# Kernel tuning notes

Hardware: AMD Instinct MI355X
Metric: run time of the kernel (lower is better)

The kernel has to match this reference:

```python
import jax, jax.numpy as jnp
import numpy as np

B, T, C, H = 4, 2048, 2048, 16
D = C // H  # head dim = 128


def setup_inputs() -> dict:
    key = jax.random.key(0)
    k1, k2, k3, k4 = jax.random.split(key, 4)
    x = jax.random.normal(k1, (B, T, C), dtype=jnp.float32)
    # per-token key mask; force token 0 valid so no causal row is fully masked
    tok_mask = jax.random.randint(k2, (B, T), 0, 2).astype(bool).at[:, 0].set(True)
    s = 1.0 / np.sqrt(C).astype(np.float32)
    W_qkv = jax.random.normal(k3, (C, 3 * C), dtype=jnp.float32) * s
    W_proj = jax.random.normal(k4, (C, C), dtype=jnp.float32) * s
    return {"x": x, "tok_mask": tok_mask, "W_qkv": W_qkv, "W_proj": W_proj}


def reference(x, tok_mask, W_qkv, W_proj):
    Bx, Tx, Cx = x.shape
    qkv = x @ W_qkv                              # [B,T,3C]
    q, k, v = jnp.split(qkv, 3, axis=-1)
    q = q.reshape(Bx, Tx, H, D)
    k = k.reshape(Bx, Tx, H, D)
    v = v.reshape(Bx, Tx, H, D)
    scale = 1.0 / np.sqrt(D).astype(np.float32)
    scores = jnp.einsum('bqhd,bkhd->bhqk', q, k) * scale  # [B,H,T,T]
    causal = jnp.tril(jnp.ones((Tx, Tx), dtype=bool))      # [T,T]
    # tok_mask broadcasts over the query dim (key mask), AND-ed with causal
    mask = tok_mask[:, None, :] & causal                   # [B,T,T]
    scores = jnp.where(mask[:, None, :, :], scores, -jnp.inf)
    attn = jax.nn.softmax(scores, axis=-1)                 # dropout p=0 -> identity
    y = jnp.einsum('bhqk,bkhd->bqhd', attn, v).reshape(Bx, Tx, Cx)
    return y @ W_proj
```

## Files before the change

kernel.cpp:

```cpp
#include <hip/hip_runtime.h>
#include <hip/hip_bf16.h>
#include <stdint.h>

typedef __bf16 bf16;
typedef __bf16 bf16x8 __attribute__((ext_vector_type(8)));
typedef float f32x4 __attribute__((ext_vector_type(4)));
typedef unsigned short u16;
typedef unsigned int u32;

constexpr int NB = 4;
constexpr int NT = 2048;
constexpr int NC = 2048;
constexpr int NH = 16;
constexpr int ND = 128;
constexpr int NC3 = 6144;

__device__ __forceinline__ void gload16(const void* g, void* l) {
  __builtin_amdgcn_global_load_lds((const __attribute__((address_space(1))) void*)g,
                                   (__attribute__((address_space(3))) void*)l, 16, 0, 0);
}

__device__ __forceinline__ u32 pack_bf16(float a, float b) {
  return (u32)__builtin_bit_cast(u16, (bf16)a) | ((u32)__builtin_bit_cast(u16, (bf16)b) << 16);
}

__global__ __launch_bounds__(256) void ingest_k(const float* __restrict__ raw, bf16* __restrict__ out, long n) {
  long i = ((long)blockIdx.x * 256 + threadIdx.x) * 8;
  if (i >= n) return;
  f32x4 a = *(const f32x4*)(raw + i), b = *(const f32x4*)(raw + i + 4);
  bf16x8 o;
  o[0] = (bf16)a[0]; o[1] = (bf16)a[1]; o[2] = (bf16)a[2]; o[3] = (bf16)a[3];
  o[4] = (bf16)b[0]; o[5] = (bf16)b[1]; o[6] = (bf16)b[2]; o[7] = (bf16)b[3];
  *(bf16x8*)(out + i) = o;
}

__global__ void mask_prep_k(const void* raw, int* out) {
  __shared__ int s_gt1, s_oddnz, s_allb, s_allf, s_allh;
  if (threadIdx.x == 0) { s_gt1 = 0; s_oddnz = 0; s_allb = 1; s_allf = 1; s_allh = 1; }
  __syncthreads();
  const unsigned int* mw = (const unsigned int*)raw;
  int gt1 = 0, oddnz = 0, allb = 1, allf = 1, allh = 1;
  for (int i = threadIdx.x; i < 2048; i += 256) {
    unsigned v = mw[i];
    if (v > 1u) gt1 = 1;
    if ((i & 1) && v) oddnz = 1;
#pragma unroll
    for (int bb = 0; bb < 4; ++bb) { unsigned by = (v >> (8*bb)) & 0xffu; if (by > 1u) allb = 0; }
    if (v != 0u && v != 0x3F800000u) allf = 0;
    unsigned lo = v & 0xffffu, hi = v >> 16;
    if ((lo != 0u && lo != 0x3F80u) || (hi != 0u && hi != 0x3F80u)) allh = 0;
  }
  if (gt1) atomicOr(&s_gt1, 1);
  if (oddnz) atomicOr(&s_oddnz, 1);
  if (!allb) atomicAnd(&s_allb, 0);
  if (!allf) atomicAnd(&s_allf, 0);
  if (!allh) atomicAnd(&s_allh, 0);
  __syncthreads();
  int mode;
  if (!s_gt1)       mode = s_oddnz ? 0 : 2;
  else if (s_allf)  mode = 3;
  else if (s_allb)  mode = 1;
  else if (s_allh)  mode = 4;
  else              mode = 0;
  for (int i = threadIdx.x; i < NB*NT; i += 256) {
    int v;
    if (mode == 0)      v = (((const int*)raw)[i] != 0);
    else if (mode == 1) v = (((const unsigned char*)raw)[i] != 0);
    else if (mode == 2) v = (((const long long*)raw)[i] != 0);
    else if (mode == 3) v = (((const unsigned int*)raw)[i] != 0);
    else                v = (((const unsigned short*)raw)[i] != 0);
    out[i] = v;
  }
}

__global__ __launch_bounds__(256) void transpose_f32_k(const float* __restrict__ in, bf16* __restrict__ out,
                                                       int in_rs, int out_rs) {
  __shared__ __align__(16) bf16 t[64][72];
  const int r0 = blockIdx.y << 6, c0 = blockIdx.x << 6;
  const int tid = threadIdx.x;
#pragma unroll
  for (int i = 0; i < 4; ++i) {
    int slot = i*256 + tid, row = slot >> 4, c4 = slot & 15;
    f32x4 v = *(const f32x4*)(in + (long)(r0 + row)*in_rs + c0 + c4*4);
#pragma unroll
    for (int e = 0; e < 4; ++e) t[c4*4 + e][row] = (bf16)v[e];
  }
  __syncthreads();
#pragma unroll
  for (int i = 0; i < 2; ++i) {
    int slot = i*256 + tid, row = slot >> 3, c8 = slot & 7;
    bf16x8 v = *(const bf16x8*)(&t[row][c8*8]);
    *(bf16x8*)(out + (long)(c0 + row)*out_rs + r0 + c8*8) = v;
  }
}

__global__ __launch_bounds__(256) void vtrans_k(const bf16* __restrict__ qkv, bf16* __restrict__ vt) {
  __shared__ __align__(16) bf16 t[64][72];
  const int tt = blockIdx.x, dh = blockIdx.y, bh = blockIdx.z;
  const int b = bh >> 4, h = bh & 15;
  const int tid = threadIdx.x;
  const bf16* src = qkv + (long)(b*NT + tt*64)*NC3 + (2*NC + h*ND + dh*64);
#pragma unroll
  for (int i = 0; i < 2; ++i) {
    int slot = i*256 + tid, row = slot >> 3, c8 = slot & 7;
    bf16x8 v = *(const bf16x8*)(src + (long)row*NC3 + c8*8);
#pragma unroll
    for (int e = 0; e < 8; ++e) t[c8*8 + e][row] = v[e];
  }
  __syncthreads();
  bf16* dst = vt + ((long)bh*ND + dh*64)*NT + tt*64;
#pragma unroll
  for (int i = 0; i < 2; ++i) {
    int slot = i*256 + tid, row = slot >> 3, c8 = slot & 7;
    bf16x8 v = *(const bf16x8*)(&t[row][c8*8]);
    *(bf16x8*)(dst + (long)row*NT + c8*8) = v;
  }
}

template <typename OT>
__global__ __launch_bounds__(256, 2) void gemm_bt_k(const bf16* __restrict__ A, const bf16* __restrict__ BT,
                                                    OT* __restrict__ Cout, int M, int N, int K) {
  const int tid = threadIdx.x, w = tid >> 6, l = tid & 63, g = l >> 4, r = l & 15;
  const int wr = w >> 1, wc = w & 1;
  const long m0 = (long)blockIdx.y << 7, n0 = (long)blockIdx.x << 7;
  __shared__ __align__(16) char As[16384];
  __shared__ __align__(16) char Bs[16384];

  long aoff[4], boff[4];
  char *al_[4], *bl_[4];
#pragma unroll
  for (int i = 0; i < 4; ++i) {
    int slot = i*256 + tid, row = slot >> 3, c = slot & 7, cp = c ^ (row & 7);
    aoff[i] = (m0 + row)*(long)K + cp*8;
    boff[i] = (n0 + row)*(long)K + cp*8;
    al_[i] = As + ((i*256 + w*64) << 4);
    bl_[i] = Bs + ((i*256 + w*64) << 4);
  }

  const f32x4 z4 = {0.f, 0.f, 0.f, 0.f};
  f32x4 acc[4][4];
#pragma unroll
  for (int mc = 0; mc < 4; ++mc)
#pragma unroll
    for (int nc = 0; nc < 4; ++nc) acc[mc][nc] = z4;

  for (int k0 = 0; k0 < K; k0 += 64) {
#pragma unroll
    for (int i = 0; i < 4; ++i) {
      gload16(A + aoff[i] + k0, al_[i]);
      gload16(BT + boff[i] + k0, bl_[i]);
    }
    __syncthreads();
#pragma unroll
    for (int kk = 0; kk < 2; ++kk) {
      bf16x8 af[4], bfr[4];
#pragma unroll
      for (int mc = 0; mc < 4; ++mc) {
        int row = wr*64 + mc*16 + r;
        af[mc] = *(const bf16x8*)(As + row*128 + (((kk*4 + g) ^ (row & 7)) << 4));
      }
#pragma unroll
      for (int nc = 0; nc < 4; ++nc) {
        int row = wc*64 + nc*16 + r;
        bfr[nc] = *(const bf16x8*)(Bs + row*128 + (((kk*4 + g) ^ (row & 7)) << 4));
      }
#pragma unroll
      for (int mc = 0; mc < 4; ++mc)
#pragma unroll
        for (int nc = 0; nc < 4; ++nc)
          acc[mc][nc] = __builtin_amdgcn_mfma_f32_16x16x32_bf16(af[mc], bfr[nc], acc[mc][nc], 0, 0, 0);
    }
    __syncthreads();
  }
#pragma unroll
  for (int mc = 0; mc < 4; ++mc)
#pragma unroll
    for (int nc = 0; nc < 4; ++nc)
#pragma unroll
      for (int j = 0; j < 4; ++j) {
        long mr = m0 + wr*64 + mc*16 + 4*g + j;
        long nc_ = n0 + wc*64 + nc*16 + r;
        Cout[mr*(long)N + nc_] = (OT)acc[mc][nc][j];
      }
}

__global__ __launch_bounds__(256, 2) void attn_k(const bf16* __restrict__ qkv, const bf16* __restrict__ vt,
                                                 const int* __restrict__ mask, bf16* __restrict__ y) {
  const int qx = blockIdx.x, h = blockIdx.y, b = blockIdx.z;
  const int qt = (qx & 1) ? (31 - (qx >> 1)) : (qx >> 1);
  const int tid = threadIdx.x, w = tid >> 6, l = tid & 63, g = l >> 4, r = l & 15;
  const int q0 = qt << 6;
  const int bh = b*NH + h;
  const int ntiles = qt + 1;
  const int qrow = q0 + w*16 + r;

  __shared__ __align__(16) char Klds[2][16384];
  __shared__ __align__(16) char Vlds[2][16384];
  __shared__ __align__(16) char Plds[8192];
  __shared__ char Mc[2048];
  char* Pl = Plds + (w << 11);

  for (int i = tid; i < q0 + 64; i += 256) Mc[i] = (char)(mask[b*NT + i] != 0);

  long koff[4], voff[4];
  int klo[4];
#pragma unroll
  for (int i = 0; i < 4; ++i) {
    int slot = i*256 + tid;
    int row = slot >> 4, c = slot & 15, cp = c ^ (row & 7);
    koff[i] = (long)row*NC3 + cp*8;
    klo[i] = (i*256 + w*64) << 4;
    int vrow = slot >> 3, vc = slot & 7, vcp = vc ^ (vrow & 7);
    voff[i] = (long)vrow*NT + vcp*8;
  }
  const bf16* kbase0 = qkv + (long)(b*NT)*NC3 + (NC + h*ND);
  const bf16* vbase0 = vt + (long)bh*ND*NT;

  bf16x8 qf[4];
  {
    const bf16* qp = qkv + (long)(b*NT + qrow)*NC3 + h*ND + g*8;
#pragma unroll
    for (int dk = 0; dk < 4; ++dk) qf[dk] = *(const bf16x8*)(qp + dk*32);
  }

  const f32x4 z4 = {0.f, 0.f, 0.f, 0.f};
  f32x4 acc[8];
#pragma unroll
  for (int i = 0; i < 8; ++i) acc[i] = z4;
  float m_run = 0.0f;
  float l_run = 0.0f;

  const float SCL = 0.08838834764831845f * 1.4426950408889634f;

#pragma unroll
  for (int i = 0; i < 4; ++i) {
    gload16(kbase0 + koff[i], Klds[0] + klo[i]);
    gload16(vbase0 + voff[i], Vlds[0] + klo[i]);
  }
  __syncthreads();

  for (int kt = 0; kt < ntiles; ++kt) {
    const int cur = kt & 1;
    if (kt + 1 < ntiles) {
      const bf16* kb = kbase0 + (long)((kt+1)*64)*NC3;
      const bf16* vb = vbase0 + (kt+1)*64;
#pragma unroll
      for (int i = 0; i < 4; ++i) {
        gload16(kb + koff[i], Klds[cur^1] + klo[i]);
        gload16(vb + voff[i], Vlds[cur^1] + klo[i]);
      }
    }
    const char* Kl = Klds[cur];
    const char* Vl = Vlds[cur];
    const int key0 = kt*64;
    const bool act = (key0 <= q0 + w*16 + 15);

    if (act) {
      u32 mw_[4];
#pragma unroll
      for (int kc = 0; kc < 4; ++kc) mw_[kc] = *(const u32*)(Mc + key0 + kc*16 + 4*g);

      float tv[4][4];
      __builtin_amdgcn_s_setprio(1);
#pragma unroll
      for (int kc = 0; kc < 4; ++kc) {
        const int krow = kc*16 + r;
        f32x4 s = z4;
#pragma unroll
        for (int dk = 0; dk < 4; ++dk) {
          bf16x8 kf = *(const bf16x8*)(Kl + krow*256 + (((dk*4 + g) ^ (krow & 7)) << 4));
          s = __builtin_amdgcn_mfma_f32_16x16x32_bf16(kf, qf[dk], s, 0, 0, 0);
        }
#pragma unroll
        for (int j = 0; j < 4; ++j) {
          const int key = key0 + kc*16 + 4*g + j;
          const bool ok = ((mw_[kc] >> (8*j)) & 0xffu) && (key <= qrow);
          tv[kc][j] = ok ? s[j]*SCL : -3.0e38f;
        }
      }
      __builtin_amdgcn_s_setprio(0);

      float tmax = -3.0e38f;
#pragma unroll
      for (int kc = 0; kc < 4; ++kc)
#pragma unroll
        for (int j = 0; j < 4; ++j) tmax = fmaxf(tmax, tv[kc][j]);
      tmax = fmaxf(tmax, __shfl_xor(tmax, 16));
      tmax = fmaxf(tmax, __shfl_xor(tmax, 32));

      if (!__all(tmax <= m_run + 8.0f)) {
        float mn = fmaxf(m_run, tmax);
        float al = exp2f(m_run - mn);
        m_run = mn;
        l_run *= al;
        float alj[4];
#pragma unroll
        for (int j = 0; j < 4; ++j) alj[j] = __shfl(al, 4*g + j);
#pragma unroll
        for (int d0 = 0; d0 < 8; ++d0)
#pragma unroll
          for (int j = 0; j < 4; ++j) acc[d0][j] *= alj[j];
      }

      float rs = 0.f;
      u32 pk0[4], pk1[4];
#pragma unroll
      for (int kc = 0; kc < 4; ++kc) {
        float p0 = exp2f(tv[kc][0] - m_run), p1 = exp2f(tv[kc][1] - m_run);
        float p2 = exp2f(tv[kc][2] - m_run), p3 = exp2f(tv[kc][3] - m_run);
        rs += (p0 + p1) + (p2 + p3);
        pk0[kc] = pack_bf16(p0, p1);
        pk1[kc] = pack_bf16(p2, p3);
      }
      rs += __shfl_xor(rs, 16);
      rs += __shfl_xor(rs, 32);
      l_run += rs;
#pragma unroll
      for (int kc = 0; kc < 4; ++kc) {
        const int off = (kc*32 + g*8) ^ ((r & 7) << 4);
        uint2 wv; wv.x = pk0[kc]; wv.y = pk1[kc];
        *(uint2*)(Pl + r*128 + off) = wv;
      }
      asm volatile("s_waitcnt lgkmcnt(0)" ::: "memory");
      __builtin_amdgcn_sched_barrier(0);
      bf16x8 pa[2];
#pragma unroll
      for (int kk = 0; kk < 2; ++kk)
        pa[kk] = *(const bf16x8*)(Pl + r*128 + ((kk*64 + g*16) ^ ((r & 7) << 4)));

      __builtin_amdgcn_s_setprio(1);
#pragma unroll
      for (int d0 = 0; d0 < 8; ++d0) {
        const int vrow = d0*16 + r;
#pragma unroll
        for (int kk = 0; kk < 2; ++kk) {
          bf16x8 vf = *(const bf16x8*)(Vl + vrow*128 + (((kk*4 + g) ^ (vrow & 7)) << 4));
          acc[d0] = __builtin_amdgcn_mfma_f32_16x16x32_bf16(pa[kk], vf, acc[d0], 0, 0, 0);
        }
      }
      __builtin_amdgcn_s_setprio(0);
    }
    __syncthreads();
  }

  float lr[4];
#pragma unroll
  for (int j = 0; j < 4; ++j) lr[j] = __shfl(l_run, 4*g + j);
#pragma unroll
  for (int d0 = 0; d0 < 8; ++d0)
#pragma unroll
    for (int j = 0; j < 4; ++j) {
      int qr = q0 + w*16 + 4*g + j;
      y[(long)(b*NT + qr)*NC + h*ND + d0*16 + r] = (bf16)(acc[d0][j] / lr[j]);
    }
}

extern "C" void kernel_launch(void* const* d_in, const int* in_sizes, int n_in,
                              void* d_out, int out_size, void* d_ws, size_t ws_size,
                              hipStream_t stream) {
  const float* xr     = (const float*)d_in[0];
  const void*  tok    = d_in[1];
  const float* wqkvr  = (const float*)d_in[2];
  const float* wprojr = (const float*)d_in[3];
  float* out = (float*)d_out;
  char* ws = (char*)d_ws;

  bf16* qkv    = (bf16*)(ws);
  bf16* yattn  = (bf16*)(ws + 100663296L);
  bf16* wT     = (bf16*)(ws + 134217728L);
  bf16* wpT    = (bf16*)(ws + 159383552L);
  bf16* xb     = (bf16*)(ws + 167772160L);
  bf16* vtb    = xb;
  int*  maskI  = (int*)(ws + 201326592L);

  mask_prep_k<<<1, 256, 0, stream>>>(tok, maskI);
  ingest_k<<<8192, 256, 0, stream>>>(xr, xb, 16777216L);
  transpose_f32_k<<<dim3(96, 32), 256, 0, stream>>>(wqkvr, wT, NC3, NC);
  transpose_f32_k<<<dim3(32, 32), 256, 0, stream>>>(wprojr, wpT, NC, NC);
  gemm_bt_k<bf16><<<dim3(48, 64), 256, 0, stream>>>(xb, wT, qkv, 8192, 6144, 2048);
  vtrans_k<<<dim3(32, 2, 64), 256, 0, stream>>>(qkv, vtb);
  attn_k<<<dim3(32, 16, 4), 256, 0, stream>>>(qkv, vtb, maskI, yattn);
  gemm_bt_k<float><<<dim3(16, 64), 256, 0, stream>>>(yattn, wpT, out, 8192, 2048, 2048);
}
```

Before: 603.5 us.

## Replace GEMM with 256x256 double-buffered tile kernel and grouped block swizzle

Replaces the 128x128 single-buffered bf16 GEMM with a 256x256-tile, 512-thread kernel. It double-buffers A/B in LDS so the next k-slab loads while MFMAs run on the current one, splits each k-step into four sub-phases with register fragment reuse and s_setprio, and remaps block IDs with an XCD-style swizzle. The aim is higher arithmetic intensity per byte loaded and hidden global-load latency in both the QKV and output projections. In exchange it uses 128KB of LDS per block, which limits occupancy to one block per CU despite launch_bounds(512,2). Register pressure rises with 32 accumulator tiles, and the output GEMM launches only 256 blocks.

Result: faster. 589.8 us (-2.3%).

```diff
diff --git a/kernel.cpp b/kernel.cpp
--- a/kernel.cpp
+++ b/kernel.cpp
@@ -118,69 +118,150 @@
 }
 
 template <typename OT>
-__global__ __launch_bounds__(256, 2) void gemm_bt_k(const bf16* __restrict__ A, const bf16* __restrict__ BT,
-                                                    OT* __restrict__ Cout, int M, int N, int K) {
+__global__ __launch_bounds__(512, 2) void gemm256_k(const bf16* __restrict__ A, const bf16* __restrict__ BT,
+                                                    OT* __restrict__ Cout, int M, int N, int K, int nbx) {
+  const int nwg = gridDim.x;
+  const int bid = blockIdx.x;
+  const int cpx = nwg >> 3;
+  const int swz = (bid & 7) * cpx + (bid >> 3);
+  const int bx = swz % nbx, by = swz / nbx;
+  const long m0 = (long)by << 8, n0 = (long)bx << 8;
+
   const int tid = threadIdx.x, w = tid >> 6, l = tid & 63, g = l >> 4, r = l & 15;
-  const int wr = w >> 1, wc = w & 1;
-  const long m0 = (long)blockIdx.y << 7, n0 = (long)blockIdx.x << 7;
-  __shared__ __align__(16) char As[16384];
-  __shared__ __align__(16) char Bs[16384];
+  const int wm = w >> 2, wn = w & 3;
+
+  __shared__ __align__(16) char As[2][32768];
+  __shared__ __align__(16) char Bs[2][32768];
 
   long aoff[4], boff[4];
-  char *al_[4], *bl_[4];
+  int slo[4];
 #pragma unroll
   for (int i = 0; i < 4; ++i) {
-    int slot = i*256 + tid, row = slot >> 3, c = slot & 7, cp = c ^ (row & 7);
+    int s = i*512 + tid, row = s >> 3, c = s & 7, cp = c ^ (row & 7);
     aoff[i] = (m0 + row)*(long)K + cp*8;
     boff[i] = (n0 + row)*(long)K + cp*8;
-    al_[i] = As + ((i*256 + w*64) << 4);
-    bl_[i] = Bs + ((i*256 + w*64) << 4);
+    slo[i] = (i*512 + w*64) << 4;
   }
 
   const f32x4 z4 = {0.f, 0.f, 0.f, 0.f};
-  f32x4 acc[4][4];
-#pragma unroll
-  for (int mc = 0; mc < 4; ++mc)
-#pragma unroll
-    for (int nc = 0; nc < 4; ++nc) acc[mc][nc] = z4;
-
-  for (int k0 = 0; k0 < K; k0 += 64) {
-#pragma unroll
-    for (int i = 0; i < 4; ++i) {
-      gload16(A + aoff[i] + k0, al_[i]);
-      gload16(BT + boff[i] + k0, bl_[i]);
+  f32x4 acc[8][4];
+#pragma unroll
+  for (int i = 0; i < 8; ++i)
+#pragma unroll
+    for (int j = 0; j < 4; ++j) acc[i][j] = z4;
+
+  const int nk = K >> 6;
+#pragma unroll
+  for (int i = 0; i < 4; ++i) {
+    gload16(A + aoff[i], As[0] + slo[i]);
+    gload16(BT + boff[i], Bs[0] + slo[i]);
+  }
+  __syncthreads();
+
+  bf16x8 af[8], bfr[4];
+
+  for (int t = 0; t < nk; ++t) {
+    const int cur = t & 1;
+    const char* Ac = As[cur];
+    const char* Bc = Bs[cur];
+
+#pragma unroll
+    for (int mi = 0; mi < 4; ++mi)
+#pragma unroll
+      for (int kk = 0; kk < 2; ++kk) {
+        int row = wm*128 + mi*16 + r;
+        af[mi*2+kk] = *(const bf16x8*)(Ac + row*128 + (((kk*4 + g) ^ (row & 7)) << 4));
+      }
+#pragma unroll
+    for (int ni = 0; ni < 2; ++ni)
+#pragma unroll
+      for (int kk = 0; kk < 2; ++kk) {
+        int row = wn*64 + ni*16 + r;
+        bfr[ni*2+kk] = *(const bf16x8*)(Bc + row*128 + (((kk*4 + g) ^ (row & 7)) << 4));
+      }
+    if (t + 1 < nk) {
+      const long ko = (long)(t+1) << 6;
+#pragma unroll
+      for (int i = 0; i < 4; ++i) {
+        gload16(A + aoff[i] + ko, As[cur^1] + slo[i]);
+        gload16(BT + boff[i] + ko, Bs[cur^1] + slo[i]);
+      }
     }
+    __builtin_amdgcn_s_setprio(1);
+#pragma unroll
+    for (int mi = 0; mi < 4; ++mi)
+#pragma unroll
+      for (int ni = 0; ni < 2; ++ni)
+#pragma unroll
+        for (int kk = 0; kk < 2; ++kk)
+          acc[mi][ni] = __builtin_amdgcn_mfma_f32_16x16x32_bf16(af[mi*2+kk], bfr[ni*2+kk], acc[mi][ni], 0, 0, 0);
+    __builtin_amdgcn_s_setprio(0);
+    __builtin_amdgcn_s_barrier();
+
+#pragma unroll
+    for (int mi = 0; mi < 4; ++mi)
+#pragma unroll
+      for (int kk = 0; kk < 2; ++kk) {
+        int row = wm*128 + 64 + mi*16 + r;
+        af[mi*2+kk] = *(const bf16x8*)(Ac + row*128 + (((kk*4 + g) ^ (row & 7)) << 4));
+      }
+    __builtin_amdgcn_s_setprio(1);
+#pragma unroll
+    for (int mi = 0; mi < 4; ++mi)
+#pragma unroll
+      for (int ni = 0; ni < 2; ++ni)
+#pragma unroll
+        for (int kk = 0; kk < 2; ++kk)
+          acc[4+mi][ni] = __builtin_amdgcn_mfma_f32_16x16x32_bf16(af[mi*2+kk], bfr[ni*2+kk], acc[4+mi][ni], 0, 0, 0);
+    __builtin_amdgcn_s_setprio(0);
+    __builtin_amdgcn_s_barrier();
+
+#pragma unroll
+    for (int ni = 0; ni < 2; ++ni)
+#pragma unroll
+      for (int kk = 0; kk < 2; ++kk) {
+        int row = wn*64 + 32 + ni*16 + r;
+        bfr[ni*2+kk] = *(const bf16x8*)(Bc + row*128 + (((kk*4 + g) ^ (row & 7)) << 4));
+      }
+    __builtin_amdgcn_s_setprio(1);
+#pragma unroll
+    for (int mi = 0; mi < 4; ++mi)
+#pragma unroll
+      for (int ni = 0; ni < 2; ++ni)
+#pragma unroll
+        for (int kk = 0; kk < 2; ++kk)
+          acc[4+mi][2+ni] = __builtin_amdgcn_mfma_f32_16x16x32_bf16(af[mi*2+kk], bfr[ni*2+kk], acc[4+mi][2+ni], 0, 0, 0);
+    __builtin_amdgcn_s_setprio(0);
+    __builtin_amdgcn_s_barrier();
+
+#pragma unroll
+    for (int mi = 0; mi < 4; ++mi)
+#pragma unroll
+      for (int kk = 0; kk < 2; ++kk) {
+        int row = wm*128 + mi*16 + r;
+        af[mi*2+kk] = *(const bf16x8*)(Ac + row*128 + (((kk*4 + g) ^ (row & 7)) << 4));
+      }
+    __builtin_amdgcn_s_setprio(1);
+#pragma unroll
+    for (int mi = 0; mi < 4; ++mi)
+#pragma unroll
+      for (int ni = 0; ni < 2; ++ni)
+#pragma unroll
+        for (int kk = 0; kk < 2; ++kk)
+          acc[mi][2+ni] = __builtin_amdgcn_mfma_f32_16x16x32_bf16(af[mi*2+kk], bfr[ni*2+kk], acc[mi][2+ni], 0, 0, 0);
+    __builtin_amdgcn_s_setprio(0);
     __syncthreads();
-#pragma unroll
-    for (int kk = 0; kk < 2; ++kk) {
-      bf16x8 af[4], bfr[4];
-#pragma unroll
-      for (int mc = 0; mc < 4; ++mc) {
-        int row = wr*64 + mc*16 + r;
-        af[mc] = *(const bf16x8*)(As + row*128 + (((kk*4 + g) ^ (row & 7)) << 4));
-      }
-#pragma unroll
-      for (int nc = 0; nc < 4; ++nc) {
-        int row = wc*64 + nc*16 + r;
-        bfr[nc] = *(const bf16x8*)(Bs + row*128 + (((kk*4 + g) ^ (row & 7)) << 4));
-      }
-#pragma unroll
-      for (int mc = 0; mc < 4; ++mc)
-#pragma unroll
-        for (int nc = 0; nc < 4; ++nc)
-          acc[mc][nc] = __builtin_amdgcn_mfma_f32_16x16x32_bf16(af[mc], bfr[nc], acc[mc][nc], 0, 0, 0);
-    }
-    __syncthreads();
-  }
-#pragma unroll
-  for (int mc = 0; mc < 4; ++mc)
-#pragma unroll
-    for (int nc = 0; nc < 4; ++nc)
+  }
+
+#pragma unroll
+  for (int mi = 0; mi < 8; ++mi)
+#pragma unroll
+    for (int ni = 0; ni < 4; ++ni)
 #pragma unroll
       for (int j = 0; j < 4; ++j) {
-        long mr = m0 + wr*64 + mc*16 + 4*g + j;
-        long nc_ = n0 + wc*64 + nc*16 + r;
-        Cout[mr*(long)N + nc_] = (OT)acc[mc][nc][j];
+        long mr = m0 + wm*128 + mi*16 + 4*g + j;
+        long nc = n0 + wn*64 + ni*16 + r;
+        Cout[mr*(long)N + nc] = (OT)acc[mi][ni][j];
       }
 }
 
@@ -377,8 +458,8 @@
   ingest_k<<<8192, 256, 0, stream>>>(xr, xb, 16777216L);
   transpose_f32_k<<<dim3(96, 32), 256, 0, stream>>>(wqkvr, wT, NC3, NC);
   transpose_f32_k<<<dim3(32, 32), 256, 0, stream>>>(wprojr, wpT, NC, NC);
-  gemm_bt_k<bf16><<<dim3(48, 64), 256, 0, stream>>>(xb, wT, qkv, 8192, 6144, 2048);
+  gemm256_k<bf16><<<768, 512, 0, stream>>>(xb, wT, qkv, 8192, 6144, 2048, 24);
   vtrans_k<<<dim3(32, 2, 64), 256, 0, stream>>>(qkv, vtb);
   attn_k<<<dim3(32, 16, 4), 256, 0, stream>>>(qkv, vtb, maskI, yattn);
-  gemm_bt_k<float><<<dim3(16, 64), 256, 0, stream>>>(yattn, wpT, out, 8192, 2048, 2048);
-}
+  gemm256_k<float><<<256, 512, 0, stream>>>(yattn, wpT, out, 8192, 2048, 2048, 8);
+}
```
